# Performance work log

Measured on AMD Instinct MI355X. Metric: run time of the kernel, lower is better.

The kernel has to match this reference:

```python
import jax, jax.numpy as jnp
import numpy as np
import math

B, H, S, D = 2, 16, 2048, 72
D12 = D // 12  # freq dim per head per component
L_PREFIX, L_SEQ = 576, 512
THETA_T = 100.0


def _make_freqs():
    n = H * D12
    log_min, log_max = math.log(math.pi), math.log(10.0 * math.pi)
    f = jnp.exp(jnp.linspace(log_min, log_max, n + 1)[:-1])  # (H*D12,)
    freqs = jnp.stack([f, f]).reshape(2, D12, H)
    freqs = jnp.swapaxes(freqs, -1, -2)  # (2, H, D12)
    t = THETA_T ** (-jnp.arange(n, dtype=jnp.float32) / n)
    t_freqs = t.reshape(D12, H).T  # (H, D12)
    return freqs.astype(jnp.float32), t_freqs.astype(jnp.float32)


def setup_inputs() -> dict:
    key = jax.random.key(0)
    ks = jax.random.split(key, 8)
    freqs, t_freqs = _make_freqs()
    return {
        "q": jax.random.normal(ks[0], (B, H, S, D), dtype=jnp.float32),
        "k": jax.random.normal(ks[1], (B, H, S, D), dtype=jnp.float32),
        "v": jax.random.normal(ks[2], (B, H, S, D), dtype=jnp.float32),
        "pos": jax.random.uniform(ks[3], (B, S, 2), dtype=jnp.float32),
        "pos_orig": jax.random.uniform(ks[4], (B, S, 2), dtype=jnp.float32),
        "time": jax.random.uniform(ks[5], (B, S), dtype=jnp.float32),
        "freqs": freqs,
        "t_freqs": t_freqs,
        "scale": jax.random.uniform(ks[6], (H, 1, 1), dtype=jnpp_f32()) if False else jax.random.uniform(ks[6], (H, 1, 1), dtype=jnp.float32) + 0.5,
        "l_prefix": L_PREFIX,
        "l_seq": L_SEQ,
    }


def jnp_f32():
    return jnp.float32


def _fp_rope_theta(pos, pos_orig, time, freqs, t_freqs):
    # FPRoPE.forward: theta per token, per head. (B,S,H,5*D12)
    p = jnp.stack([pos_orig, pos], axis=2) * 2.0 - 1.0  # (B,S,2,2)
    th_w = p[..., 0][:, :, :, None, None] * freqs[0]  # (B,S,2,H,D12)
    th_h = p[..., 1][:, :, :, None, None] * freqs[1]  # (B,S,2,H,D12)
    th_t = time[:, :, None, None, None] * t_freqs      # (B,S,1,H,D12)
    theta = jnp.concatenate([th_h, th_w, th_t], axis=2)  # (B,S,5,H,D12)
    theta = jnp.transpose(theta, (0, 3, 1, 2, 4)).reshape(B, H, S, 5 * D12)
    return theta


def _apply_rotary(x, theta):
    d = theta.shape[-1]
    x1, x2, x3 = x[..., :d], x[..., d:2 * d], x[..., 2 * d:]
    c, s = jnp.cos(theta), jnp.sin(theta)
    return jnp.concatenate([x1 * c - x2 * s, x2 * c + x1 * s, x3], axis=-1)


def _block_mask(l_prefix, l_seq):
    # inference_query_causal_mask_mod: prefix attends to nothing; pokes causal;
    # queries attend to prefix+pokes (and self via qn==kn).
    idx = jnp.arange(S)
    qn = (idx - l_prefix)[:, None]
    kn = (idx - l_prefix)[None, :]
    return (qn >= 0) & ((qn == kn) | ((qn >= kn) & (qn < l_seq)) | ((kn < l_seq) & (qn >= l_seq)))


def reference(q, k, v, pos, pos_orig, time, freqs, t_freqs, scale, l_prefix, l_seq):
    theta = _fp_rope_theta(pos, pos_orig, time, freqs, t_freqs)
    q = _apply_rotary(q, theta)
    k = _apply_rotary(k, theta)
    # cosine-similarity QK rescaling (scale_for_cosine_sim)
    eps = 1e-6
    ss = jnp.sqrt(scale)  # (H,1,1) broadcasts over (B,H,S,1)
    q = q * (ss * jax.lax.rsqrt(jnp.sum(q * q, axis=-1, keepdims=True) + eps))
    k = k * (ss * jax.lax.rsqrt(jnp.sum(k * k, axis=-1, keepdims=True) + eps))
    mask = _block_mask(l_prefix, l_seq)  # (S,S)
    scores = jnp.einsum('bhqd,bhkd->bhqk', q, k)
    scores = jnp.where(mask, scores, jnp.float32(-1e30))
    probs = jax.nn.softmax(scores, axis=-1)
    # fully-masked rows (prefix queries) output zeros, matching flex_attention
    row_valid = jnp.any(mask, axis=-1)  # (S,)
    probs = jnp.where(row_valid[None, None, :, None], probs, 0.0)
    return jnp.einsum('bhqk,bhkd->bhqd', probs, v)
```

## Files before the change

### kernel.cpp

```cpp
#include <hip/hip_runtime.h>
#include <math.h>

#define B_ 2
#define H_ 16
#define S_ 2048
#define D_ 72
#define LP 576
#define WEND 1088
#define DP 96
#define DV 80
#define NQ (S_ - LP)

#define KS 50
#define VS 33
#define PW 33
#define VBASE (64 * KS)
#define PBASE (VBASE + DV * VS)
#define LDSW (PBASE + 4 * 16 * PW)

#define NPREP2 (B_ * H_ * S_ / 8)
#define NVT    (32 * B_ * H_)

typedef __bf16 bf16x8 __attribute__((ext_vector_type(8)));
typedef float f32x4 __attribute__((ext_vector_type(4)));

static __device__ __forceinline__ unsigned pack2bf(float a, float b) {
    __bf16 x = (__bf16)a, y = (__bf16)b;
    unsigned short ux = __builtin_bit_cast(unsigned short, x);
    unsigned short uy = __builtin_bit_cast(unsigned short, y);
    return (unsigned)ux | ((unsigned)uy << 16);
}

static __device__ __forceinline__ f32x4 mfma16(bf16x8 a, bf16x8 b, f32x4 c) {
    return __builtin_amdgcn_mfma_f32_16x16x32_bf16(a, b, c, 0, 0, 0);
}

__global__ __launch_bounds__(256) void pre_kernel(
    const float* __restrict__ q, const float* __restrict__ k,
    const float* __restrict__ v,
    const float* __restrict__ pos, const float* __restrict__ pos_orig,
    const float* __restrict__ time_, const float* __restrict__ freqs,
    const float* __restrict__ t_freqs, const float* __restrict__ scale,
    unsigned* __restrict__ qn, unsigned* __restrict__ kn,
    unsigned short* __restrict__ vt, float* __restrict__ out)
{
    __shared__ __align__(16) float tile[64 * 77];
    if (blockIdx.x < NPREP2) {
        unsigned short* shp = (unsigned short*)tile;
        const int wave = threadIdx.x >> 6;
        const int lane = threadIdx.x & 63;
        const int j = lane & 31;
        const int rw = wave * 2 + (lane >> 5);
        const int row = blockIdx.x * 8 + rw;
        const int s = row & (S_ - 1);
        const int h = (row >> 11) & (H_ - 1);
        const int b = row >> 15;
        const long base = (long)row * D_;
        const int p2 = (b * S_ + s) * 2;

        float oq1 = 0.f, oq2 = 0.f, ok1 = 0.f, ok2 = 0.f;
        float pq[6], pk[6];
        float ssq = 0.f, ssk = 0.f;
        if (j < 30) {
            const float x1q = q[base + j], x2q = q[base + j + 30];
            const float x1k = k[base + j], x2k = k[base + j + 30];
            const int g = j / 6, i = j - 6 * g;
            const float fh = freqs[96 + h * 6 + i];
            const float fw = freqs[h * 6 + i];
            const float ft = t_freqs[h * 6 + i];
            const float f  = (g < 2) ? fh : ((g < 4) ? fw : ft);
            const float by_o = pos_orig[p2 + 1] * 2.f - 1.f;
            const float by_p = pos[p2 + 1]      * 2.f - 1.f;
            const float bx_o = pos_orig[p2 + 0] * 2.f - 1.f;
            const float bx_p = pos[p2 + 0]      * 2.f - 1.f;
            const float bt   = time_[b * S_ + s];
            const float bv = (g == 0) ? by_o : (g == 1) ? by_p :
                             (g == 2) ? bx_o : (g == 3) ? bx_p : bt;
            float sn, cs;
            __sincosf(bv * f, &sn, &cs);
            oq1 = x1q * cs - x2q * sn;  oq2 = x2q * cs + x1q * sn;
            ok1 = x1k * cs - x2k * sn;  ok2 = x2k * cs + x1k * sn;
            ssq = oq1 * oq1 + oq2 * oq2;
            ssk = ok1 * ok1 + ok2 * ok2;
        } else {
            const int e0 = 60 + 6 * (j - 30);
            #pragma unroll
            for (int m = 0; m < 3; ++m) {
                const float2 a = *(const float2*)(q + base + e0 + 2 * m);
                const float2 c = *(const float2*)(k + base + e0 + 2 * m);
                pq[2 * m] = a.x; pq[2 * m + 1] = a.y;
                pk[2 * m] = c.x; pk[2 * m + 1] = c.y;
                ssq += a.x * a.x + a.y * a.y;
                ssk += c.x * c.x + c.y * c.y;
            }
        }
        #pragma unroll
        for (int m = 1; m < 32; m <<= 1) { ssq += __shfl_xor(ssq, m); ssk += __shfl_xor(ssk, m); }
        const float ss = sqrtf(scale[h]);
        const float fq = ss * rsqrtf(ssq + 1e-6f);
        const float fk = ss * rsqrtf(ssk + 1e-6f);

        unsigned short* sq_ = shp + rw * 96;
        unsigned short* sk_ = shp + 768 + rw * 96;
        if (j < 30) {
            sq_[j]      = __builtin_bit_cast(unsigned short, (__bf16)(oq1 * fq));
            sq_[j + 30] = __builtin_bit_cast(unsigned short, (__bf16)(oq2 * fq));
            sk_[j]      = __builtin_bit_cast(unsigned short, (__bf16)(ok1 * fk));
            sk_[j + 30] = __builtin_bit_cast(unsigned short, (__bf16)(ok2 * fk));
        } else {
            const int e0 = 60 + 6 * (j - 30);
            #pragma unroll
            for (int m = 0; m < 6; ++m) {
                sq_[e0 + m] = __builtin_bit_cast(unsigned short, (__bf16)(pq[m] * fq));
                sk_[e0 + m] = __builtin_bit_cast(unsigned short, (__bf16)(pk[m] * fk));
            }
        }
        __syncthreads();
        const int t = threadIdx.x;
        if (t < 192) {
            const int arr = t / 96, rem = t - arr * 96;
            const int rr = rem / 12, seg = rem - rr * 12;
            uint4 val = make_uint4(0u, 0u, 0u, 0u);
            if (seg < 9) val = ((const uint4*)(shp + arr * 768 + rr * 96))[seg];
            unsigned* dst = (arr ? kn : qn) + ((long)(blockIdx.x * 8 + rr)) * 48;
            ((uint4*)dst)[seg] = val;
        }
    } else {
        const int bx2 = blockIdx.x - NPREP2;
        const int st = bx2 & 31, bh = bx2 >> 5;
        const int s0 = st * 64;
        const int t = threadIdx.x;
        if (st < 9) {
            float4* o4 = (float4*)(out + (long)(bh * S_ + s0) * D_);
            for (int i = t; i < 1152; i += 256) o4[i] = make_float4(0.f, 0.f, 0.f, 0.f);
        }
        for (int i = t; i < 1152; i += 256) {
            const int r = i / 18, c = i - r * 18;
            const float4 g = ((const float4*)v)[((long)(bh * S_ + s0 + r) * 18) + c];
            float* d = &tile[r * 77 + c * 4];
            d[0] = g.x; d[1] = g.y; d[2] = g.z; d[3] = g.w;
        }
        __syncthreads();
        for (int i = t; i < 1280; i += 256) {
            const int dd = i >> 4, s4 = i & 15;
            float f0 = 0.f, f1 = 0.f, f2 = 0.f, f3 = 0.f;
            if (dd < D_) {
                f0 = tile[(s4 * 4 + 0) * 77 + dd];
                f1 = tile[(s4 * 4 + 1) * 77 + dd];
                f2 = tile[(s4 * 4 + 2) * 77 + dd];
                f3 = tile[(s4 * 4 + 3) * 77 + dd];
            }
            uint2 o; o.x = pack2bf(f0, f1); o.y = pack2bf(f2, f3);
            ((uint2*)vt)[((((long)bh * DV + dd) << 11) + s0 + s4 * 4) >> 2] = o;
        }
    }
}

__global__ __launch_bounds__(256) void attn_kernel(
    const unsigned short* __restrict__ qn, const unsigned short* __restrict__ kn,
    const unsigned short* __restrict__ vt,
    float* __restrict__ po, float* __restrict__ pden)
{
    __shared__ __align__(16) unsigned lds[LDSW];
    const int bh = blockIdx.y;
    const int kz = blockIdx.z;
    const int q0 = LP + blockIdx.x * 64;
    const int tid = threadIdx.x;
    const int w = tid >> 6, lane = tid & 63;
    const int quad = lane >> 4, l16 = lane & 15;
    const int q0w = q0 + 16 * w;
    const bool causal = (q0 < WEND);
    const int ntiles = causal ? (q0 >> 6) + 1 : (WEND >> 6);

    const unsigned short* qn_b = qn + (((long)bh) << 11) * DP;
    const unsigned short* kn_b = kn + (((long)bh) << 11) * DP;
    const unsigned short* vt_b = vt + (long)bh * DV * S_;

    bf16x8 qf[3];
    #pragma unroll
    for (int c = 0; c < 3; ++c)
        qf[c] = *(const bf16x8*)(qn_b + (long)(q0w + l16) * DP + c * 32 + quad * 8);

    f32x4 o[5];
    float den[4];
    #pragma unroll
    for (int dt = 0; dt < 5; ++dt) { o[dt][0]=0.f; o[dt][1]=0.f; o[dt][2]=0.f; o[dt][3]=0.f; }
    #pragma unroll
    for (int r = 0; r < 4; ++r) den[r] = 0.f;

    unsigned* Ps = lds + PBASE + w * (16 * PW);

    for (int kt = kz; kt < ntiles; kt += 2) {
        const int k0 = kt * 64;
        __syncthreads();
        #pragma unroll
        for (int ii = 0; ii < 3; ++ii) {
            const int i = tid + ii * 256;
            const int r = i / 12, seg = i - r * 12;
            const int key = k0 + 32 * (r >> 5) + 2 * (r & 15) + ((r >> 4) & 1);
            *(uint4*)(lds + r * KS + seg * 4) = *(const uint4*)(kn_b + (long)key * DP + seg * 8);
        }
        for (int i = tid; i < 640; i += 256) {
            const int rr = i >> 3, seg = i & 7;
            *(uint4*)(lds + VBASE + rr * VS + seg * 4) =
                *(const uint4*)(vt_b + (((long)rr) << 11) + k0 + seg * 8);
        }
        __syncthreads();

        f32x4 acc[4];
        #pragma unroll
        for (int G = 0; G < 4; ++G) { acc[G][0]=0.f; acc[G][1]=0.f; acc[G][2]=0.f; acc[G][3]=0.f; }
        #pragma unroll
        for (int c = 0; c < 3; ++c)
            #pragma unroll
            for (int G = 0; G < 4; ++G) {
                const bf16x8 kf = *(const bf16x8*)(lds + (16 * G + l16) * KS + c * 16 + quad * 4);
                acc[G] = mfma16(qf[c], kf, acc[G]);
            }
        #pragma unroll
        for (int g2 = 0; g2 < 2; ++g2) {
            const int kb = k0 + 32 * g2 + 2 * l16;
            #pragma unroll
            for (int r = 0; r < 4; ++r) {
                const int qa = q0w + quad * 4 + r;
                float p0 = acc[2 * g2][r], p1 = acc[2 * g2 + 1][r];
                p0 = (!causal || kb     <= qa) ? __expf(p0) : 0.f;
                p1 = (!causal || kb + 1 <= qa) ? __expf(p1) : 0.f;
                const __bf16 pb0 = (__bf16)p0, pb1 = (__bf16)p1;
                den[r] += (float)pb0 + (float)pb1;
                Ps[(quad * 4 + r) * PW + g2 * 16 + l16] =
                    (unsigned)__builtin_bit_cast(unsigned short, pb0) |
                    ((unsigned)__builtin_bit_cast(unsigned short, pb1) << 16);
            }
        }
        const bf16x8 pa0 = *(const bf16x8*)(Ps + l16 * PW + quad * 4);
        const bf16x8 pa1 = *(const bf16x8*)(Ps + l16 * PW + 16 + quad * 4);
        #pragma unroll
        for (int dt = 0; dt < 5; ++dt) {
            const bf16x8 vf0 = *(const bf16x8*)(lds + VBASE + (dt * 16 + l16) * VS + quad * 4);
            const bf16x8 vf1 = *(const bf16x8*)(lds + VBASE + (dt * 16 + l16) * VS + 16 + quad * 4);
            o[dt] = mfma16(pa0, vf0, o[dt]);
            o[dt] = mfma16(pa1, vf1, o[dt]);
        }
    }

    #pragma unroll
    for (int r = 0; r < 4; ++r)
        #pragma unroll
        for (int x = 1; x < 16; x <<= 1) den[r] += __shfl_xor(den[r], x);

    if (kz == 1 && !causal) {
        float* PsD = (float*)Ps;
        float sp = 0.f;
        #pragma unroll
        for (int c = 0; c < 3; ++c) {
            const bf16x8 kd = *(const bf16x8*)(kn_b + (long)(q0w + l16) * DP + c * 32 + quad * 8);
            #pragma unroll
            for (int j = 0; j < 8; ++j) sp += (float)qf[c][j] * (float)kd[j];
        }
        sp += __shfl_xor(sp, 16);
        sp += __shfl_xor(sp, 32);
        if (quad == 0) PsD[l16] = __expf(sp);
        #pragma unroll
        for (int r = 0; r < 4; ++r) {
            const float pd = PsD[quad * 4 + r];
            den[r] += pd;
            const int qa = q0w + quad * 4 + r;
            #pragma unroll
            for (int dt = 0; dt < 5; ++dt) {
                const unsigned short uv = vt_b[(((long)(dt * 16 + l16)) << 11) + qa];
                o[dt][r] += pd * (float)__builtin_bit_cast(__bf16, uv);
            }
        }
    }

    const long pobase = ((long)(kz * 32 + bh)) * NQ * DV;
    const long pdbase = ((long)(kz * 32 + bh)) * NQ;
    #pragma unroll
    for (int r = 0; r < 4; ++r) {
        const int rq = blockIdx.x * 64 + 16 * w + quad * 4 + r;
        #pragma unroll
        for (int dt = 0; dt < 5; ++dt)
            po[pobase + (long)rq * DV + dt * 16 + l16] = o[dt][r];
        if (l16 == 0) pden[pdbase + rq] = den[r];
    }
}

__global__ __launch_bounds__(256) void combine_kernel(
    const float* __restrict__ po, const float* __restrict__ pden,
    float* __restrict__ out)
{
    const int t = threadIdx.x;
    const int rowid = blockIdx.x * 16 + (t >> 4);
    const int d0 = t & 15;
    const int bh = rowid / NQ;
    const int rq = rowid - bh * NQ;
    const long p0 = ((long)bh) * NQ * DV + (long)rq * DV;
    const long p1 = ((long)(32 + bh)) * NQ * DV + (long)rq * DV;
    const float den = pden[(long)bh * NQ + rq] + pden[(long)(32 + bh) * NQ + rq];
    const float inv = 1.f / den;
    float* orow = out + ((long)bh * S_ + LP + rq) * D_;
    #pragma unroll
    for (int j = 0; j < 5; ++j) {
        const int d = d0 + 16 * j;
        if (d < D_) orow[d] = (po[p0 + d] + po[p1 + d]) * inv;
    }
}

extern "C" void kernel_launch(void* const* d_in, const int* in_sizes, int n_in,
                              void* d_out, int out_size, void* d_ws, size_t ws_size,
                              hipStream_t stream) {
    const float* q        = (const float*)d_in[0];
    const float* k        = (const float*)d_in[1];
    const float* v        = (const float*)d_in[2];
    const float* pos      = (const float*)d_in[3];
    const float* pos_orig = (const float*)d_in[4];
    const float* time_    = (const float*)d_in[5];
    const float* freqs    = (const float*)d_in[6];
    const float* t_freqs  = (const float*)d_in[7];
    const float* scale    = (const float*)d_in[8];
    float* out = (float*)d_out;

    unsigned* qn = (unsigned*)d_ws;
    unsigned* kn = qn + (size_t)B_ * H_ * S_ * 48;
    unsigned short* vt = (unsigned short*)(kn + (size_t)B_ * H_ * S_ * 48);
    float* po = (float*)(vt + (size_t)B_ * H_ * DV * S_);
    float* pden = po + (size_t)2 * B_ * H_ * NQ * DV;

    pre_kernel<<<dim3(NPREP2 + NVT), dim3(256), 0, stream>>>(
        q, k, v, pos, pos_orig, time_, freqs, t_freqs, scale, qn, kn, vt, out);
    attn_kernel<<<dim3(NQ / 64, B_ * H_, 2), dim3(256), 0, stream>>>(
        (const unsigned short*)qn, (const unsigned short*)kn, vt, po, pden);
    combine_kernel<<<dim3(B_ * H_ * NQ / 16), dim3(256), 0, stream>>>(po, pden, out);
}
```

Before: 199.3 us.

## Drop split-K and combine kernel; give each wave two query tiles

The attention kernel no longer splits the key range across two blocks, so the partial output and denominator buffers and the separate combine kernel are removed. Each block now runs 128 threads (two waves) and writes the normalized output directly. Each wave handles 32 query rows as two 16-row MFMA tiles, so every K and V fragment loaded from LDS is reused twice. The aim is to cut global traffic for the partial results and one kernel launch, and to improve data reuse. The cost is half as many blocks and waves, with longer sequential key loops per block, which lowers parallelism and makes the causal load imbalance worse.

New measurement: 240.4 us. 1.21x slower.

```diff
diff --git a/kernel.cpp b/kernel.cpp
--- a/kernel.cpp
+++ b/kernel.cpp
@@ -16,7 +16,7 @@
 #define PW 33
 #define VBASE (64 * KS)
 #define PBASE (VBASE + DV * VS)
-#define LDSW (PBASE + 4 * 16 * PW)
+#define LDSW (PBASE + 2 * 16 * PW)
 
 #define NPREP2 (B_ * H_ * S_ / 8)
 #define NVT    (32 * B_ * H_)
@@ -156,155 +156,158 @@
     }
 }
 
-__global__ __launch_bounds__(256) void attn_kernel(
+__global__ __launch_bounds__(128, 3) void attn_kernel(
     const unsigned short* __restrict__ qn, const unsigned short* __restrict__ kn,
-    const unsigned short* __restrict__ vt,
-    float* __restrict__ po, float* __restrict__ pden)
+    const unsigned short* __restrict__ vt, float* __restrict__ out)
 {
     __shared__ __align__(16) unsigned lds[LDSW];
     const int bh = blockIdx.y;
-    const int kz = blockIdx.z;
     const int q0 = LP + blockIdx.x * 64;
     const int tid = threadIdx.x;
     const int w = tid >> 6, lane = tid & 63;
     const int quad = lane >> 4, l16 = lane & 15;
-    const int q0w = q0 + 16 * w;
+    const int q0w = q0 + 32 * w;
     const bool causal = (q0 < WEND);
-    const int ntiles = causal ? (q0 >> 6) + 1 : (WEND >> 6);
+    const int ntiles = causal ? ((q0 + 63) >> 6) + 1 : (WEND >> 6);
 
     const unsigned short* qn_b = qn + (((long)bh) << 11) * DP;
     const unsigned short* kn_b = kn + (((long)bh) << 11) * DP;
     const unsigned short* vt_b = vt + (long)bh * DV * S_;
 
-    bf16x8 qf[3];
+    bf16x8 qf[2][3];
     #pragma unroll
-    for (int c = 0; c < 3; ++c)
-        qf[c] = *(const bf16x8*)(qn_b + (long)(q0w + l16) * DP + c * 32 + quad * 8);
-
-    f32x4 o[5];
-    float den[4];
+    for (int m = 0; m < 2; ++m)
+        #pragma unroll
+        for (int c = 0; c < 3; ++c)
+            qf[m][c] = *(const bf16x8*)(qn_b + (long)(q0w + m * 16 + l16) * DP + c * 32 + quad * 8);
+
+    f32x4 o[2][5];
+    float den[2][4];
     #pragma unroll
-    for (int dt = 0; dt < 5; ++dt) { o[dt][0]=0.f; o[dt][1]=0.f; o[dt][2]=0.f; o[dt][3]=0.f; }
-    #pragma unroll
-    for (int r = 0; r < 4; ++r) den[r] = 0.f;
+    for (int m = 0; m < 2; ++m) {
+        #pragma unroll
+        for (int dt = 0; dt < 5; ++dt) { o[m][dt][0]=0.f; o[m][dt][1]=0.f; o[m][dt][2]=0.f; o[m][dt][3]=0.f; }
+        #pragma unroll
+        for (int r = 0; r < 4; ++r) den[m][r] = 0.f;
+    }
 
     unsigned* Ps = lds + PBASE + w * (16 * PW);
 
-    for (int kt = kz; kt < ntiles; kt += 2) {
+    for (int kt = 0; kt < ntiles; ++kt) {
         const int k0 = kt * 64;
         __syncthreads();
         #pragma unroll
-        for (int ii = 0; ii < 3; ++ii) {
-            const int i = tid + ii * 256;
+        for (int ii = 0; ii < 6; ++ii) {
+            const int i = tid + ii * 128;
             const int r = i / 12, seg = i - r * 12;
             const int key = k0 + 32 * (r >> 5) + 2 * (r & 15) + ((r >> 4) & 1);
             *(uint4*)(lds + r * KS + seg * 4) = *(const uint4*)(kn_b + (long)key * DP + seg * 8);
         }
-        for (int i = tid; i < 640; i += 256) {
+        #pragma unroll
+        for (int ii = 0; ii < 5; ++ii) {
+            const int i = tid + ii * 128;
             const int rr = i >> 3, seg = i & 7;
             *(uint4*)(lds + VBASE + rr * VS + seg * 4) =
                 *(const uint4*)(vt_b + (((long)rr) << 11) + k0 + seg * 8);
         }
         __syncthreads();
 
-        f32x4 acc[4];
-        #pragma unroll
-        for (int G = 0; G < 4; ++G) { acc[G][0]=0.f; acc[G][1]=0.f; acc[G][2]=0.f; acc[G][3]=0.f; }
+        f32x4 acc[2][4];
+        #pragma unroll
+        for (int m = 0; m < 2; ++m)
+            #pragma unroll
+            for (int G = 0; G < 4; ++G) { acc[m][G][0]=0.f; acc[m][G][1]=0.f; acc[m][G][2]=0.f; acc[m][G][3]=0.f; }
         #pragma unroll
         for (int c = 0; c < 3; ++c)
             #pragma unroll
             for (int G = 0; G < 4; ++G) {
                 const bf16x8 kf = *(const bf16x8*)(lds + (16 * G + l16) * KS + c * 16 + quad * 4);
-                acc[G] = mfma16(qf[c], kf, acc[G]);
-            }
-        #pragma unroll
-        for (int g2 = 0; g2 < 2; ++g2) {
-            const int kb = k0 + 32 * g2 + 2 * l16;
-            #pragma unroll
-            for (int r = 0; r < 4; ++r) {
-                const int qa = q0w + quad * 4 + r;
-                float p0 = acc[2 * g2][r], p1 = acc[2 * g2 + 1][r];
-                p0 = (!causal || kb     <= qa) ? __expf(p0) : 0.f;
-                p1 = (!causal || kb + 1 <= qa) ? __expf(p1) : 0.f;
-                const __bf16 pb0 = (__bf16)p0, pb1 = (__bf16)p1;
-                den[r] += (float)pb0 + (float)pb1;
-                Ps[(quad * 4 + r) * PW + g2 * 16 + l16] =
-                    (unsigned)__builtin_bit_cast(unsigned short, pb0) |
-                    ((unsigned)__builtin_bit_cast(unsigned short, pb1) << 16);
-            }
-        }
-        const bf16x8 pa0 = *(const bf16x8*)(Ps + l16 * PW + quad * 4);
-        const bf16x8 pa1 = *(const bf16x8*)(Ps + l16 * PW + 16 + quad * 4);
+                acc[0][G] = mfma16(qf[0][c], kf, acc[0][G]);
+                acc[1][G] = mfma16(qf[1][c], kf, acc[1][G]);
+            }
+        bf16x8 pa[2][2];
+        #pragma unroll
+        for (int m = 0; m < 2; ++m) {
+            #pragma unroll
+            for (int g2 = 0; g2 < 2; ++g2) {
+                const int kb = k0 + 32 * g2 + 2 * l16;
+                #pragma unroll
+                for (int r = 0; r < 4; ++r) {
+                    const int qa = q0w + m * 16 + quad * 4 + r;
+                    float p0 = acc[m][2 * g2][r], p1 = acc[m][2 * g2 + 1][r];
+                    p0 = (!causal || kb     <= qa) ? __expf(p0) : 0.f;
+                    p1 = (!causal || kb + 1 <= qa) ? __expf(p1) : 0.f;
+                    const __bf16 pb0 = (__bf16)p0, pb1 = (__bf16)p1;
+                    den[m][r] += (float)pb0 + (float)pb1;
+                    Ps[(quad * 4 + r) * PW + g2 * 16 + l16] =
+                        (unsigned)__builtin_bit_cast(unsigned short, pb0) |
+                        ((unsigned)__builtin_bit_cast(unsigned short, pb1) << 16);
+                }
+            }
+            pa[m][0] = *(const bf16x8*)(Ps + l16 * PW + quad * 4);
+            pa[m][1] = *(const bf16x8*)(Ps + l16 * PW + 16 + quad * 4);
+        }
         #pragma unroll
         for (int dt = 0; dt < 5; ++dt) {
             const bf16x8 vf0 = *(const bf16x8*)(lds + VBASE + (dt * 16 + l16) * VS + quad * 4);
             const bf16x8 vf1 = *(const bf16x8*)(lds + VBASE + (dt * 16 + l16) * VS + 16 + quad * 4);
-            o[dt] = mfma16(pa0, vf0, o[dt]);
-            o[dt] = mfma16(pa1, vf1, o[dt]);
+            o[0][dt] = mfma16(pa[0][0], vf0, o[0][dt]);
+            o[0][dt] = mfma16(pa[0][1], vf1, o[0][dt]);
+            o[1][dt] = mfma16(pa[1][0], vf0, o[1][dt]);
+            o[1][dt] = mfma16(pa[1][1], vf1, o[1][dt]);
         }
     }
 
     #pragma unroll
-    for (int r = 0; r < 4; ++r)
-        #pragma unroll
-        for (int x = 1; x < 16; x <<= 1) den[r] += __shfl_xor(den[r], x);
-
-    if (kz == 1 && !causal) {
+    for (int m = 0; m < 2; ++m)
+        #pragma unroll
+        for (int r = 0; r < 4; ++r)
+            #pragma unroll
+            for (int x = 1; x < 16; x <<= 1) den[m][r] += __shfl_xor(den[m][r], x);
+
+    if (!causal) {
         float* PsD = (float*)Ps;
-        float sp = 0.f;
-        #pragma unroll
-        for (int c = 0; c < 3; ++c) {
-            const bf16x8 kd = *(const bf16x8*)(kn_b + (long)(q0w + l16) * DP + c * 32 + quad * 8);
-            #pragma unroll
-            for (int j = 0; j < 8; ++j) sp += (float)qf[c][j] * (float)kd[j];
-        }
-        sp += __shfl_xor(sp, 16);
-        sp += __shfl_xor(sp, 32);
-        if (quad == 0) PsD[l16] = __expf(sp);
+        #pragma unroll
+        for (int m = 0; m < 2; ++m) {
+            float sp = 0.f;
+            #pragma unroll
+            for (int c = 0; c < 3; ++c) {
+                const bf16x8 kd = *(const bf16x8*)(kn_b + (long)(q0w + m * 16 + l16) * DP + c * 32 + quad * 8);
+                #pragma unroll
+                for (int j = 0; j < 8; ++j) sp += (float)qf[m][c][j] * (float)kd[j];
+            }
+            sp += __shfl_xor(sp, 16);
+            sp += __shfl_xor(sp, 32);
+            if (quad == 0) PsD[m * 16 + l16] = __expf(sp);
+        }
+        #pragma unroll
+        for (int m = 0; m < 2; ++m)
+            #pragma unroll
+            for (int r = 0; r < 4; ++r) {
+                const float pd = PsD[m * 16 + quad * 4 + r];
+                den[m][r] += pd;
+                const int qa = q0w + m * 16 + quad * 4 + r;
+                #pragma unroll
+                for (int dt = 0; dt < 5; ++dt) {
+                    const unsigned short uv = vt_b[(((long)(dt * 16 + l16)) << 11) + qa];
+                    o[m][dt][r] += pd * (float)__builtin_bit_cast(__bf16, uv);
+                }
+            }
+    }
+
+    #pragma unroll
+    for (int m = 0; m < 2; ++m)
         #pragma unroll
         for (int r = 0; r < 4; ++r) {
-            const float pd = PsD[quad * 4 + r];
-            den[r] += pd;
-            const int qa = q0w + quad * 4 + r;
+            const float inv = 1.f / den[m][r];
+            const int qa = q0w + m * 16 + quad * 4 + r;
+            float* orow = out + ((long)(bh * S_ + qa)) * D_;
             #pragma unroll
             for (int dt = 0; dt < 5; ++dt) {
-                const unsigned short uv = vt_b[(((long)(dt * 16 + l16)) << 11) + qa];
-                o[dt][r] += pd * (float)__builtin_bit_cast(__bf16, uv);
-            }
-        }
-    }
-
-    const long pobase = ((long)(kz * 32 + bh)) * NQ * DV;
-    const long pdbase = ((long)(kz * 32 + bh)) * NQ;
-    #pragma unroll
-    for (int r = 0; r < 4; ++r) {
-        const int rq = blockIdx.x * 64 + 16 * w + quad * 4 + r;
-        #pragma unroll
-        for (int dt = 0; dt < 5; ++dt)
-            po[pobase + (long)rq * DV + dt * 16 + l16] = o[dt][r];
-        if (l16 == 0) pden[pdbase + rq] = den[r];
-    }
-}
-
-__global__ __launch_bounds__(256) void combine_kernel(
-    const float* __restrict__ po, const float* __restrict__ pden,
-    float* __restrict__ out)
-{
-    const int t = threadIdx.x;
-    const int rowid = blockIdx.x * 16 + (t >> 4);
-    const int d0 = t & 15;
-    const int bh = rowid / NQ;
-    const int rq = rowid - bh * NQ;
-    const long p0 = ((long)bh) * NQ * DV + (long)rq * DV;
-    const long p1 = ((long)(32 + bh)) * NQ * DV + (long)rq * DV;
-    const float den = pden[(long)bh * NQ + rq] + pden[(long)(32 + bh) * NQ + rq];
-    const float inv = 1.f / den;
-    float* orow = out + ((long)bh * S_ + LP + rq) * D_;
-    #pragma unroll
-    for (int j = 0; j < 5; ++j) {
-        const int d = d0 + 16 * j;
-        if (d < D_) orow[d] = (po[p0 + d] + po[p1 + d]) * inv;
-    }
+                const int dim = dt * 16 + l16;
+                if (dim < D_) orow[dim] = o[m][dt][r] * inv;
+            }
+        }
 }
 
 extern "C" void kernel_launch(void* const* d_in, const int* in_sizes, int n_in,
@@ -324,12 +327,9 @@
     unsigned* qn = (unsigned*)d_ws;
     unsigned* kn = qn + (size_t)B_ * H_ * S_ * 48;
     unsigned short* vt = (unsigned short*)(kn + (size_t)B_ * H_ * S_ * 48);
-    float* po = (float*)(vt + (size_t)B_ * H_ * DV * S_);
-    float* pden = po + (size_t)2 * B_ * H_ * NQ * DV;
 
     pre_kernel<<<dim3(NPREP2 + NVT), dim3(256), 0, stream>>>(
         q, k, v, pos, pos_orig, time_, freqs, t_freqs, scale, qn, kn, vt, out);
-    attn_kernel<<<dim3(NQ / 64, B_ * H_, 2), dim3(256), 0, stream>>>(
-        (const unsigned short*)qn, (const unsigned short*)kn, vt, po, pden);
-    combine_kernel<<<dim3(B_ * H_ * NQ / 16), dim3(256), 0, stream>>>(po, pden, out);
-}
+    attn_kernel<<<dim3(NQ / 64, B_ * H_), dim3(128), 0, stream>>>(
+        (const unsigned short*)qn, (const unsigned short*)kn, vt, out);
+}
```
